# Performance work log

Measured on AMD Instinct MI355X. Metric: run time of the kernel, lower is better.

The kernel has to match this reference:

```python
import jax, jax.numpy as jnp
import numpy as np

HIDDEN = 1024
HEADS = 16
HEAD_DIM = HIDDEN // HEADS
LN_EPS = 1e-12


def _layer_norm(x, gamma, beta, eps=LN_EPS):
    mu = jnp.mean(x, axis=-1, keepdims=True)
    var = jnp.var(x, axis=-1, keepdims=True)
    return (x - mu) * jax.lax.rsqrt(var + eps) * gamma + beta


def setup_inputs() -> dict:
    key = jax.random.key(0)
    ks = jax.random.split(key, 8)
    B, S = 4, 2048
    hidden_states = jax.random.normal(ks[0], (B, S, HIDDEN), dtype=jnp.float32)
    attention_mask = jnp.zeros((B, 1, 1, S), dtype=jnp.float32)
    scale = 1.0 / np.sqrt(HIDDEN)
    return {
        "hidden_states": hidden_states,
        "attention_mask": attention_mask,
        "ln_gamma": jnp.ones((HIDDEN,), jnp.float32),
        "ln_beta": jnp.zeros((HIDDEN,), jnp.float32),
        "W_qkv": jax.random.normal(ks[1], (HIDDEN, 3 * HIDDEN), jnp.float32) * scale,
        "b_qkv": jnp.zeros((3 * HIDDEN,), jnp.float32),
        "W_out": jax.random.normal(ks[2], (HIDDEN, HIDDEN), jnp.float32) * scale,
        "b_out": jnp.zeros((HIDDEN,), jnp.float32),
    }


def reference(hidden_states, attention_mask, ln_gamma, ln_beta, W_qkv, b_qkv, W_out, b_out):
    B, S, H = hidden_states.shape
    x = _layer_norm(hidden_states, ln_gamma, ln_beta)
    qkv = x @ W_qkv + b_qkv  # [B, S, 3H]
    q, k, v = jnp.split(qkv, 3, axis=-1)
    q = q.reshape(B, S, HEADS, HEAD_DIM)
    k = k.reshape(B, S, HEADS, HEAD_DIM)
    v = v.reshape(B, S, HEADS, HEAD_DIM)
    # scores: [B, heads, q_len, kv_len]
    scores = jnp.einsum("bqhd,bkhd->bhqk", q, k) * (1.0 / np.sqrt(HEAD_DIM))
    scores = scores + attention_mask
    probs = jax.nn.softmax(scores, axis=-1)
    attn = jnp.einsum("bhqk,bkhd->bqhd", probs, v).reshape(B, S, H)
    out = attn @ W_out + b_out
    out = out + hidden_states  # residual (dropout is identity at p=0)
    return out
```

## Files before the change

### kernel.cpp

```cpp
#include <hip/hip_runtime.h>

#define SEQ 2048
#define HID 1024
#define NHEAD 16
#define HDIM 64
#define NB 4
#define NTOK (NB * SEQ)
#define NQKV (3 * HID)
#define LOG2E 1.44269504088896f
#define QSCALE (0.125f * LOG2E)

typedef __attribute__((ext_vector_type(8))) short bf16x8;
typedef __attribute__((ext_vector_type(4))) float f32x4;


__device__ __forceinline__ void glds16(const void* g, void* l) {
  __builtin_amdgcn_global_load_lds(
      (const __attribute__((address_space(1))) void*)g,
      (__attribute__((address_space(3))) void*)l, 16, 0, 0);
}

__device__ __forceinline__ ushort f2bf(float f) {
  union { float f; unsigned int u; } a; a.f = f;
  unsigned int u = a.u;
  return (ushort)((u + 0x7fffu + ((u >> 16) & 1u)) >> 16);
}

__device__ __forceinline__ unsigned int pack2bf_rh(float a, float b) {
  return __builtin_amdgcn_perm(__float_as_uint(b) + 0x8000u,
                               __float_as_uint(a) + 0x8000u, 0x07060302u);
}


__global__ __launch_bounds__(256) void ln_kernel(const float* __restrict__ x,
                                                 const float* __restrict__ g,
                                                 const float* __restrict__ be,
                                                 ushort* __restrict__ y) {
  const int row = blockIdx.x;
  const int tid = threadIdx.x;
  const float4 v = ((const float4*)(x + (size_t)row * HID))[tid];
  float s  = v.x + v.y + v.z + v.w;
  float sq = v.x * v.x + v.y * v.y + v.z * v.z + v.w * v.w;
  for (int o = 1; o < 64; o <<= 1) { s += __shfl_xor(s, o, 64); sq += __shfl_xor(sq, o, 64); }
  __shared__ float as_[4], aq_[4];
  const int wv = tid >> 6;
  if ((tid & 63) == 0) { as_[wv] = s; aq_[wv] = sq; }
  __syncthreads();
  s  = as_[0] + as_[1] + as_[2] + as_[3];
  sq = aq_[0] + aq_[1] + aq_[2] + aq_[3];
  const float mu  = s * (1.0f / HID);
  const float var = sq * (1.0f / HID) - mu * mu;
  const float rs  = rsqrtf(var + 1e-12f);
  const float4 gv = ((const float4*)g)[tid];
  const float4 bv = ((const float4*)be)[tid];
  ushort4 o;
  o.x = f2bf((v.x - mu) * rs * gv.x + bv.x);
  o.y = f2bf((v.y - mu) * rs * gv.y + bv.y);
  o.z = f2bf((v.z - mu) * rs * gv.z + bv.z);
  o.w = f2bf((v.w - mu) * rs * gv.w + bv.w);
  ((ushort4*)(y + (size_t)row * HID))[tid] = o;
}


__global__ __launch_bounds__(256) void mask_scale(const float* __restrict__ m,
                                                  float* __restrict__ o) {
  const int i = blockIdx.x * 256 + threadIdx.x;
  o[i] = m[i] * LOG2E;
}


__global__ __launch_bounds__(256) void transpose_cvt(const float* __restrict__ W,
                                                     ushort* __restrict__ WT,
                                                     int R, int C) {
  __shared__ float t[32][33];
  const int c0 = blockIdx.x * 32, r0 = blockIdx.y * 32;
  const int tx = threadIdx.x & 31, ty = threadIdx.x >> 5;
  for (int j = 0; j < 4; ++j)
    t[ty + j * 8][tx] = W[(size_t)(r0 + ty + j * 8) * C + c0 + tx];
  __syncthreads();
  for (int j = 0; j < 4; ++j)
    WT[(size_t)(c0 + ty + j * 8) * R + r0 + tx] = f2bf(t[tx][ty + j * 8]);
}


__global__ __launch_bounds__(256) void v_transpose(const ushort* __restrict__ qkv,
                                                   ushort* __restrict__ vt) {
  __shared__ ushort t[64][66];
  const int s0 = blockIdx.x * 64, h = blockIdx.y, b = blockIdx.z;
  const size_t tokbase = (size_t)b * SEQ;
  for (int e = 0; e < 2; ++e) {
    const int c = e * 256 + threadIdx.x;
    const int sr = c >> 3, dc = c & 7;
    *(uint4*)&t[sr][dc * 8] =
        *(const uint4*)(qkv + (tokbase + s0 + sr) * NQKV + 2 * HID + h * HDIM + dc * 8);
  }
  __syncthreads();
  for (int e = 0; e < 2; ++e) {
    const int c = e * 256 + threadIdx.x;
    const int dr = c >> 3, sc = c & 7;
    ushort tmp[8];
    for (int j = 0; j < 8; ++j) tmp[j] = t[sc * 8 + j][dr];
    *(uint4*)(vt + ((size_t)(b * NHEAD + h) * HDIM + dr) * SEQ + s0 + sc * 8) = *(uint4*)tmp;
  }
}


template <int MODE>
__global__ __launch_bounds__(256) void gemm_bt(const ushort* __restrict__ A,
                                               const ushort* __restrict__ Bt,
                                               const float* __restrict__ bias,
                                               const float* __restrict__ resid,
                                               ushort* __restrict__ obf,
                                               float* __restrict__ of32,
                                               int M, int N, int K) {
  __shared__ ushort As[128 * 64];
  __shared__ ushort Bs[128 * 64];
  const int tid = threadIdx.x;
  const int lane = tid & 63, wv = tid >> 6;
  const int q = lane >> 4, li = lane & 15;
  const int m0 = blockIdx.y * 128, n0 = blockIdx.x * 128;
  const int wm = (wv >> 1) * 64, wn = (wv & 1) * 64;
  f32x4 acc[4][4] = {};

  for (int kb = 0; kb < K; kb += 64) {
    for (int e = 0; e < 4; ++e) {
      const int chunk = (wv * 4 + e) * 64 + lane;
      const int row = chunk >> 3, slot = chunk & 7;
      const int kc = slot ^ (row & 7);
      glds16(A  + (size_t)(m0 + row) * K + kb + kc * 8, As + (wv * 4 + e) * 512);
      glds16(Bt + (size_t)(n0 + row) * K + kb + kc * 8, Bs + (wv * 4 + e) * 512);
    }
    __syncthreads();
    for (int ks = 0; ks < 2; ++ks) {
      const int kc = ks * 4 + q;
      bf16x8 af[4], bfr[4];
      for (int mi = 0; mi < 4; ++mi) {
        const int row = wm + mi * 16 + li;
        af[mi] = *(const bf16x8*)(As + (row * 8 + (kc ^ (row & 7))) * 8);
      }
      for (int ni = 0; ni < 4; ++ni) {
        const int row = wn + ni * 16 + li;
        bfr[ni] = *(const bf16x8*)(Bs + (row * 8 + (kc ^ (row & 7))) * 8);
      }
      for (int mi = 0; mi < 4; ++mi)
        for (int ni = 0; ni < 4; ++ni)
          acc[mi][ni] = __builtin_amdgcn_mfma_f32_16x16x32_bf16(af[mi], bfr[ni], acc[mi][ni], 0, 0, 0);
    }
    __syncthreads();
  }

  const float qs = (MODE == 0 && n0 < HID) ? QSCALE : 1.0f;
  for (int ni = 0; ni < 4; ++ni) {
    const int col = n0 + wn + ni * 16 + li;
    const float bvs = bias[col] * qs;
    for (int mi = 0; mi < 4; ++mi) {
      for (int r = 0; r < 4; ++r) {
        const int row = m0 + wm + mi * 16 + q * 4 + r;
        const float v = fmaf(acc[mi][ni][r], qs, bvs);
        if (MODE == 0) obf[(size_t)row * N + col] = f2bf(v);
        else           of32[(size_t)row * N + col] = v + resid[(size_t)row * N + col];
      }
    }
  }
}


__global__ __launch_bounds__(256) void flash_attn(const ushort* __restrict__ qkv,
                                                  const ushort* __restrict__ vt,
                                                  const float* __restrict__ mask2,
                                                  ushort* __restrict__ outa) {
  __shared__ ushort KV[2][8192];
  __shared__ float Ml[SEQ];
  const int tid = threadIdx.x, lane = tid & 63, wv = tid >> 6;
  const int quad = lane >> 4, li = lane & 15;
  const int wq = wv * 32;
  const int qt = blockIdx.x, h = blockIdx.y, b = blockIdx.z;
  const size_t tokbase = (size_t)b * SEQ;
  const size_t vtbase = (size_t)(b * NHEAD + h) * HDIM * SEQ;

  for (int e = 0; e < 4; ++e) {
    const int c = (wv * 4 + e) * 64 + lane;
    const int row = c >> 3, slot = c & 7;
    const int kc = slot ^ (row & 7);
    glds16(qkv + (tokbase + qt * 128 + row) * NQKV + h * HDIM + kc * 8,
           &KV[0][0] + (wv * 4 + e) * 512);
  }
  for (int e = 0; e < 2; ++e) {
    const int c = (wv * 2 + e) * 64 + lane;
    glds16(mask2 + (size_t)b * SEQ + c * 4, Ml + (wv * 2 + e) * 256);
  }
  __syncthreads();

  bf16x8 qf[2][2];
  for (int ks = 0; ks < 2; ++ks) {
    const int kc = ks * 4 + quad;
    for (int nq = 0; nq < 2; ++nq) {
      const int row = wq + nq * 16 + li;
      qf[ks][nq] = *(const bf16x8*)(&KV[0][0] + (row * 8 + (kc ^ (row & 7))) * 8);
    }
  }
  __syncthreads();

  f32x4 accO[2][4] = {};
  float l_st[2] = {0.f, 0.f};

  auto stage_kv = [&](int t, int buf) {
    const int kv0 = t * 64;
    ushort* Kb = &KV[buf][0];
    ushort* Vb = &KV[buf][4096];
    for (int e = 0; e < 2; ++e) {
      const int c = (wv * 2 + e) * 64 + lane;
      const int row = c >> 3, slot = c & 7;
      const int kc = slot ^ (row & 7);
      const int gkv = (row & 0x23) | ((row & 0x0c) << 1) | ((row & 0x10) >> 2);
      glds16(qkv + (tokbase + kv0 + gkv) * NQKV + HID + h * HDIM + kc * 8,
             Kb + (wv * 2 + e) * 512);
      glds16(vt + vtbase + (size_t)row * SEQ + kv0 + kc * 8,
             Vb + (wv * 2 + e) * 512);
    }
  };

  auto compute = [&](int t, int buf) {
    const int kv0 = t * 64;
    const ushort* Kb = &KV[buf][0];
    const ushort* Vb = &KV[buf][4096];

    float4 mk[4];
    for (int mkv = 0; mkv < 4; ++mkv)
      mk[mkv] = *(const float4*)(Ml + kv0 + (mkv >> 1) * 32 + quad * 8 + (mkv & 1) * 4);
    f32x4 sc[2][4];
    for (int nq = 0; nq < 2; ++nq)
      for (int mkv = 0; mkv < 4; ++mkv) {
        sc[nq][mkv][0] = mk[mkv].x; sc[nq][mkv][1] = mk[mkv].y;
        sc[nq][mkv][2] = mk[mkv].z; sc[nq][mkv][3] = mk[mkv].w;
      }
    for (int ks = 0; ks < 2; ++ks) {
      const int kc = ks * 4 + quad;
      bf16x8 kf[4];
      for (int mkv = 0; mkv < 4; ++mkv) {
        const int row = mkv * 16 + li;
        kf[mkv] = *(const bf16x8*)(Kb + (row * 8 + (kc ^ (row & 7))) * 8);
      }
      for (int nq = 0; nq < 2; ++nq)
        for (int mkv = 0; mkv < 4; ++mkv)
          sc[nq][mkv] = __builtin_amdgcn_mfma_f32_16x16x32_bf16(kf[mkv], qf[ks][nq], sc[nq][mkv], 0, 0, 0);
    }

    unsigned int pk[2][4][2];
    for (int nq = 0; nq < 2; ++nq) {
      float rsum = 0.f;
      for (int mkv = 0; mkv < 4; ++mkv) {
        const float p0 = __builtin_amdgcn_exp2f(sc[nq][mkv][0]);
        const float p1 = __builtin_amdgcn_exp2f(sc[nq][mkv][1]);
        const float p2 = __builtin_amdgcn_exp2f(sc[nq][mkv][2]);
        const float p3 = __builtin_amdgcn_exp2f(sc[nq][mkv][3]);
        rsum += (p0 + p1) + (p2 + p3);
        pk[nq][mkv][0] = pack2bf_rh(p0, p1);
        pk[nq][mkv][1] = pack2bf_rh(p2, p3);
      }
      rsum += __shfl_xor(rsum, 16, 64);
      rsum += __shfl_xor(rsum, 32, 64);
      l_st[nq] += rsum;
    }

    for (int ks = 0; ks < 2; ++ks) {
      const int kc = ks * 4 + quad;
      bf16x8 vf[4];
      for (int nd = 0; nd < 4; ++nd) {
        const int row = nd * 16 + li;
        vf[nd] = *(const bf16x8*)(Vb + (row * 8 + (kc ^ (row & 7))) * 8);
      }
      for (int mq = 0; mq < 2; ++mq) {
        bf16x8 pf;
        ((unsigned int*)&pf)[0] = pk[mq][2 * ks][0];
        ((unsigned int*)&pf)[1] = pk[mq][2 * ks][1];
        ((unsigned int*)&pf)[2] = pk[mq][2 * ks + 1][0];
        ((unsigned int*)&pf)[3] = pk[mq][2 * ks + 1][1];
        for (int nd = 0; nd < 4; ++nd)
          accO[mq][nd] = __builtin_amdgcn_mfma_f32_16x16x32_bf16(pf, vf[nd], accO[mq][nd], 0, 0, 0);
      }
    }
  };

  stage_kv(0, 0);
  for (int t = 0; t < SEQ / 64; t += 2) {
    __syncthreads();
    stage_kv(t + 1, 1);
    compute(t, 0);
    __syncthreads();
    if (t + 2 < SEQ / 64) stage_kv(t + 2, 0);
    compute(t + 1, 1);
  }

  for (int mq = 0; mq < 2; ++mq)
    for (int r = 0; r < 4; ++r) {
      const float lv = __shfl(l_st[mq], (lane & 48) | (quad * 4 + r), 64);
      const float inv = 1.0f / lv;
      const size_t tok = tokbase + qt * 128 + wq + mq * 16 + quad * 4 + r;
      for (int nd = 0; nd < 4; ++nd)
        outa[tok * HID + h * HDIM + nd * 16 + li] = f2bf(accO[mq][nd][r] * inv);
    }
}


extern "C" void kernel_launch(void* const* d_in, const int* in_sizes, int n_in,
                              void* d_out, int out_size, void* d_ws, size_t ws_size,
                              hipStream_t stream) {
  const float* hidden = (const float*)d_in[0];
  const float* mask   = (const float*)d_in[1];
  const float* gamma  = (const float*)d_in[2];
  const float* beta   = (const float*)d_in[3];
  const float* Wqkv   = (const float*)d_in[4];
  const float* bqkv   = (const float*)d_in[5];
  const float* Wout   = (const float*)d_in[6];
  const float* bout   = (const float*)d_in[7];
  float* out = (float*)d_out;

  char* ws = (char*)d_ws;
  ushort* x_bf  = (ushort*)(ws);
  ushort* vtb   = (ushort*)(ws);
  ushort* wqkvT = (ushort*)(ws + ((size_t)16 << 20));
  float*  mask2 = (float*) (ws + ((size_t)16 << 20));
  ushort* woutT = (ushort*)(ws + ((size_t)22 << 20));
  ushort* qkvb  = (ushort*)(ws + ((size_t)24 << 20));
  ushort* attnb = (ushort*)(ws + ((size_t)72 << 20));

  ln_kernel<<<NTOK, 256, 0, stream>>>(hidden, gamma, beta, x_bf);
  transpose_cvt<<<dim3(NQKV / 32, HID / 32), 256, 0, stream>>>(Wqkv, wqkvT, HID, NQKV);
  transpose_cvt<<<dim3(HID / 32, HID / 32), 256, 0, stream>>>(Wout, woutT, HID, HID);
  gemm_bt<0><<<dim3(NQKV / 128, NTOK / 128), 256, 0, stream>>>(
      x_bf, wqkvT, bqkv, nullptr, qkvb, nullptr, NTOK, NQKV, HID);
  mask_scale<<<(NB * SEQ) / 256, 256, 0, stream>>>(mask, mask2);
  v_transpose<<<dim3(SEQ / 64, NHEAD, NB), 256, 0, stream>>>(qkvb, vtb);
  flash_attn<<<dim3(SEQ / 128, NHEAD, NB), 256, 0, stream>>>(qkvb, vtb, mask2, attnb);
  gemm_bt<1><<<dim3(HID / 128, NTOK / 128), 256, 0, stream>>>(
      attnb, woutT, bout, hidden, nullptr, out, NTOK, HID, HID);
}
```

Before: 305.2 us.

## Fuse mask scaling into attention and remap blocks for XCD locality

Removes the separate mask_scale kernel and its staging of the mask into shared memory. flash_attn now reads the raw mask from global memory and folds the LOG2E scale in with an fma before exp2. The block index is also remapped so that the 16 query tiles of one (batch, head) pair run on the same XCD and can share K/V in that XCD's L2. In exchange there are extra global mask loads inside the inner loop, and the shared-memory footprint drops.

After: 307.6 us. About the same (+0.8%).

```diff
diff --git a/kernel.cpp b/kernel.cpp
--- a/kernel.cpp
+++ b/kernel.cpp
@@ -59,13 +59,6 @@
   o.z = f2bf((v.z - mu) * rs * gv.z + bv.z);
   o.w = f2bf((v.w - mu) * rs * gv.w + bv.w);
   ((ushort4*)(y + (size_t)row * HID))[tid] = o;
-}
-
-
-__global__ __launch_bounds__(256) void mask_scale(const float* __restrict__ m,
-                                                  float* __restrict__ o) {
-  const int i = blockIdx.x * 256 + threadIdx.x;
-  o[i] = m[i] * LOG2E;
 }
 
 
@@ -167,16 +160,21 @@
 
 __global__ __launch_bounds__(256) void flash_attn(const ushort* __restrict__ qkv,
                                                   const ushort* __restrict__ vt,
-                                                  const float* __restrict__ mask2,
+                                                  const float* __restrict__ mask,
                                                   ushort* __restrict__ outa) {
   __shared__ ushort KV[2][8192];
-  __shared__ float Ml[SEQ];
   const int tid = threadIdx.x, lane = tid & 63, wv = tid >> 6;
   const int quad = lane >> 4, li = lane & 15;
   const int wq = wv * 32;
-  const int qt = blockIdx.x, h = blockIdx.y, b = blockIdx.z;
+
+  const int L = blockIdx.x + 16 * blockIdx.y + 256 * blockIdx.z;
+  const int xcd = L & 7, rrem = L >> 3;
+  const int p = (rrem >> 4) * 8 + xcd;
+  const int qt = rrem & 15, h = p & 15, b = p >> 4;
+
   const size_t tokbase = (size_t)b * SEQ;
   const size_t vtbase = (size_t)(b * NHEAD + h) * HDIM * SEQ;
+  const float* mrow = mask + (size_t)b * SEQ;
 
   for (int e = 0; e < 4; ++e) {
     const int c = (wv * 4 + e) * 64 + lane;
@@ -184,10 +182,6 @@
     const int kc = slot ^ (row & 7);
     glds16(qkv + (tokbase + qt * 128 + row) * NQKV + h * HDIM + kc * 8,
            &KV[0][0] + (wv * 4 + e) * 512);
-  }
-  for (int e = 0; e < 2; ++e) {
-    const int c = (wv * 2 + e) * 64 + lane;
-    glds16(mask2 + (size_t)b * SEQ + c * 4, Ml + (wv * 2 + e) * 256);
   }
   __syncthreads();
 
@@ -227,13 +221,9 @@
 
     float4 mk[4];
     for (int mkv = 0; mkv < 4; ++mkv)
-      mk[mkv] = *(const float4*)(Ml + kv0 + (mkv >> 1) * 32 + quad * 8 + (mkv & 1) * 4);
-    f32x4 sc[2][4];
-    for (int nq = 0; nq < 2; ++nq)
-      for (int mkv = 0; mkv < 4; ++mkv) {
-        sc[nq][mkv][0] = mk[mkv].x; sc[nq][mkv][1] = mk[mkv].y;
-        sc[nq][mkv][2] = mk[mkv].z; sc[nq][mkv][3] = mk[mkv].w;
-      }
+      mk[mkv] = *(const float4*)(mrow + kv0 + (mkv >> 1) * 32 + quad * 8 + (mkv & 1) * 4);
+
+    f32x4 sc[2][4] = {};
     for (int ks = 0; ks < 2; ++ks) {
       const int kc = ks * 4 + quad;
       bf16x8 kf[4];
@@ -250,10 +240,10 @@
     for (int nq = 0; nq < 2; ++nq) {
       float rsum = 0.f;
       for (int mkv = 0; mkv < 4; ++mkv) {
-        const float p0 = __builtin_amdgcn_exp2f(sc[nq][mkv][0]);
-        const float p1 = __builtin_amdgcn_exp2f(sc[nq][mkv][1]);
-        const float p2 = __builtin_amdgcn_exp2f(sc[nq][mkv][2]);
-        const float p3 = __builtin_amdgcn_exp2f(sc[nq][mkv][3]);
+        const float p0 = __builtin_amdgcn_exp2f(fmaf(mk[mkv].x, LOG2E, sc[nq][mkv][0]));
+        const float p1 = __builtin_amdgcn_exp2f(fmaf(mk[mkv].y, LOG2E, sc[nq][mkv][1]));
+        const float p2 = __builtin_amdgcn_exp2f(fmaf(mk[mkv].z, LOG2E, sc[nq][mkv][2]));
+        const float p3 = __builtin_amdgcn_exp2f(fmaf(mk[mkv].w, LOG2E, sc[nq][mkv][3]));
         rsum += (p0 + p1) + (p2 + p3);
         pk[nq][mkv][0] = pack2bf_rh(p0, p1);
         pk[nq][mkv][1] = pack2bf_rh(p2, p3);
@@ -320,7 +310,6 @@
   ushort* x_bf  = (ushort*)(ws);
   ushort* vtb   = (ushort*)(ws);
   ushort* wqkvT = (ushort*)(ws + ((size_t)16 << 20));
-  float*  mask2 = (float*) (ws + ((size_t)16 << 20));
   ushort* woutT = (ushort*)(ws + ((size_t)22 << 20));
   ushort* qkvb  = (ushort*)(ws + ((size_t)24 << 20));
   ushort* attnb = (ushort*)(ws + ((size_t)72 << 20));
@@ -330,9 +319,8 @@
   transpose_cvt<<<dim3(HID / 32, HID / 32), 256, 0, stream>>>(Wout, woutT, HID, HID);
   gemm_bt<0><<<dim3(NQKV / 128, NTOK / 128), 256, 0, stream>>>(
       x_bf, wqkvT, bqkv, nullptr, qkvb, nullptr, NTOK, NQKV, HID);
-  mask_scale<<<(NB * SEQ) / 256, 256, 0, stream>>>(mask, mask2);
   v_transpose<<<dim3(SEQ / 64, NHEAD, NB), 256, 0, stream>>>(qkvb, vtb);
-  flash_attn<<<dim3(SEQ / 128, NHEAD, NB), 256, 0, stream>>>(qkvb, vtb, mask2, attnb);
+  flash_attn<<<dim3(SEQ / 128, NHEAD, NB), 256, 0, stream>>>(qkvb, vtb, mask, attnb);
   gemm_bt<1><<<dim3(HID / 128, NTOK / 128), 256, 0, stream>>>(
       attnb, woutT, bout, hidden, nullptr, out, NTOK, HID, HID);
 }
```
